# Kernel tuning notes

Measured on AMD Instinct MI355X. Metric: run time of the kernel, lower is better.

Reference implementation:

```python
import jax, jax.numpy as jnp
import numpy as np

BS, SL, N_AGENTS, OBS_DIM, STATE_DIM, N_EDGES, HID = 32, 512, 32, 96, 1024, 64, 256


def _hgcn(w_line, x, H):
    # x: [B, n, 1]; H: [B, n, E]. Faithful to torch HGCN:
    # A = D^{-1/2} H |W| B^{-1} H^T D^{-1/2}, with D, B built from detached H/|W|,
    # inf entries (from 0^{-1} / 0^{-0.5}) zeroed. Diagonal matmuls are implicit scalings.
    w_abs = jnp.abs(w_line)
    Hd = jax.lax.stop_gradient(H)
    d = jnp.einsum('bne,e->bn', Hd, jax.lax.stop_gradient(w_abs))  # [B, n]
    d_is = jnp.where(d > 0, jax.lax.rsqrt(jnp.where(d > 0, d, 1.0)), 0.0)
    b = jnp.sum(Hd, axis=-2)  # [B, E]
    b_inv = jnp.where(b > 0, 1.0 / jnp.where(b > 0, b, 1.0), 0.0)
    t = d_is[..., None] * x                       # D^{-1/2} x
    s = jnp.einsum('bne,bnk->bek', H, t)          # H^T (...)
    s = s * (w_abs[None, :] * b_inv)[..., None]   # |W| B^{-1} (diagonals commute)
    y = jnp.einsum('bne,bek->bnk', H, s)          # H (...)
    return d_is[..., None] * y                    # D^{-1/2} (...)


def _mlp(x, w1, b1, w2, b2):
    return jax.nn.relu(x @ w1 + b1) @ w2 + b2


def setup_inputs() -> dict:
    key = jax.random.key(0)
    ks = jax.random.split(key, 24)
    f = jax.random.normal
    inp = {
        'agent_qs': f(ks[0], (BS, SL, N_AGENTS), jnp.float32),
        'states': f(ks[1], (BS, SL, STATE_DIM), jnp.float32),
        'indiv_us': f(ks[2], (BS, SL, N_AGENTS, OBS_DIM), jnp.float32),
        'edge_W': f(ks[3], (OBS_DIM, N_EDGES), jnp.float32) * 0.1,
        'edge_b': f(ks[4], (N_EDGES,), jnp.float32) * 0.1,
        'wline1': 1.0 + 0.1 * f(ks[5], (N_EDGES,), jnp.float32),
        'wline2': 1.0 + 0.1 * f(ks[6], (N_EDGES,), jnp.float32),
    }
    names = ['hw1', 'hc1', 'hw', 'hc']
    outs = [N_AGENTS, N_AGENTS, N_AGENTS, 1]
    for i, (nm, od) in enumerate(zip(names, outs)):
        inp[nm + '_w1'] = f(ks[7 + 4 * i], (STATE_DIM, HID), jnp.float32) * 0.05
        inp[nm + '_b1'] = f(ks[8 + 4 * i], (HID,), jnp.float32) * 0.05
        inp[nm + '_w2'] = f(ks[9 + 4 * i], (HID, od), jnp.float32) * 0.05
        inp[nm + '_b2'] = f(ks[10 + 4 * i], (od,), jnp.float32) * 0.05
    return inp


def reference(agent_qs, states, indiv_us, edge_W, edge_b, wline1, wline2,
              hw1_w1, hw1_b1, hw1_w2, hw1_b2, hc1_w1, hc1_b1, hc1_w2, hc1_b2,
              hw_w1, hw_b1, hw_w2, hw_b2, hc_w1, hc_b1, hc_w2, hc_b2):
    bs, sl, n = agent_qs.shape
    q = agent_qs.reshape(-1, n)                               # [B, n]
    u = indiv_us.reshape(-1, n, indiv_us.shape[-1])           # [B, n, obs]
    s = states.reshape(-1, states.shape[-1])                  # [B, state_dim]
    H = jax.nn.relu(u @ edge_W + edge_b)                      # hyper_edge_net -> [B, n, E]
    x = q[..., None]                                          # node_features [B, n, 1]
    qs_tot = _hgcn(wline2, _hgcn(wline1, x, H), H)[..., 0]    # two stacked HGCN encoders
    w1 = jnp.abs(_mlp(s, hw1_w1, hw1_b1, hw1_w2, hw1_b2))
    c1 = _mlp(s, hc1_w1, hc1_b1, hc1_w2, hc1_b2)
    qt = jax.nn.elu(qs_tot * w1 + c1)
    w = jnp.abs(_mlp(s, hw_w1, hw_b1, hw_w2, hw_b2))
    c = _mlp(s, hc_w1, hc_b1, hc_w2, hc_b2)[..., 0]
    q_tot = jnp.sum(qt * w, axis=-1) + c
    return q_tot.reshape(bs, sl, 1)
```

## Files before the change

### kernel.cpp

```cpp
#include <hip/hip_runtime.h>
#include <cstdint>

typedef _Float16 f16;
typedef _Float16 f16x4 __attribute__((ext_vector_type(4)));
typedef _Float16 f16x8 __attribute__((ext_vector_type(8)));
typedef float f32x4 __attribute__((ext_vector_type(4)));

#define AS1U const __attribute__((address_space(1))) unsigned int
#define AS3U __attribute__((address_space(3))) unsigned int

__device__ __forceinline__ void gload_lds16(const void* g, void* l) {
    __builtin_amdgcn_global_load_lds((AS1U*)g, (AS3U*)l, 16, 0, 0);
}

#define WSYNC() asm volatile("s_waitcnt lgkmcnt(0)" ::: "memory")

#define BATCH 16384
#define NAG   32
#define OBS   96
#define SDIM  1024
#define NE    64
#define HIDN  256
#define NH    1024

#define NB_ST 1024
#define NB_PW 256
#define NB_SM 101
#define NB_HG 4096
#define NB_FRONT (NB_ST + NB_PW + NB_SM + NB_HG)

__global__ __launch_bounds__(256) void k_front(
    const float* __restrict__ agent_qs, const float* __restrict__ states,
    const float* __restrict__ indiv_us, const float* __restrict__ edge_W,
    const float* __restrict__ edge_b, const float* __restrict__ wline1,
    const float* __restrict__ wline2,
    const float* __restrict__ w1a, const float* __restrict__ w1b,
    const float* __restrict__ w1c, const float* __restrict__ w1d,
    const float* __restrict__ b1a, const float* __restrict__ b1b,
    const float* __restrict__ b1c, const float* __restrict__ b1d,
    const float* __restrict__ w2a, const float* __restrict__ w2b,
    const float* __restrict__ w2c, const float* __restrict__ w2d,
    f16* __restrict__ states16, f16* __restrict__ W1t, float* __restrict__ b1cat,
    f16* __restrict__ W2t, f16* __restrict__ hcw2, float* __restrict__ qs_tot) {
    __shared__ __align__(16) char arena[50688];
    const int tid = threadIdx.x;
    int bid = blockIdx.x;

    if (bid < NB_ST) {
        int i = bid * 256 + tid;
        const int n4 = BATCH * SDIM / 4;
        const int stride = NB_ST * 256;
        for (; i < n4; i += stride) {
            float4 v = ((const float4*)states)[i];
            f16x4 h = { (f16)v.x, (f16)v.y, (f16)v.z, (f16)v.w };
            ((f16x4*)states16)[i] = h;
        }
        return;
    }
    bid -= NB_ST;
    if (bid < NB_PW) {
        float* tile = (float*)arena;
        int mlp = bid >> 6, rem = bid & 63, kt = rem >> 2, ct = rem & 3;
        const float* src = (mlp == 0) ? w1a : (mlp == 1) ? w1b : (mlp == 2) ? w1c : w1d;
        int k0 = kt * 64, c0 = ct * 64;
        for (int i = tid; i < 4096; i += 256) {
            int kk = i >> 6, cc = i & 63;
            tile[kk * 65 + cc] = src[(size_t)(k0 + kk) * 256 + c0 + cc];
        }
        __syncthreads();
        for (int i = tid; i < 4096; i += 256) {
            int cc = i >> 6, kk = i & 63;
            W1t[(size_t)(mlp * 256 + c0 + cc) * 1024 + k0 + kk] = (f16)tile[kk * 65 + cc];
        }
        return;
    }
    bid -= NB_PW;
    if (bid < NB_SM) {
        int i = bid * 256 + tid;
        if (i < 24576) {
            int mp = i >> 13, rem = i & 8191, oo = rem >> 8, kk = rem & 255;
            const float* src = (mp == 0) ? w2a : (mp == 1) ? w2b : w2c;
            W2t[i] = (f16)src[kk * 32 + oo];
        } else if (i < 24832) {
            int k = i - 24576;
            hcw2[k] = (f16)w2d[k];
        } else {
            int n = i - 24832;
            int mlp = n >> 8, c = n & 255;
            const float* bsrc = (mlp == 0) ? b1a : (mlp == 1) ? b1b : (mlp == 2) ? b1c : b1d;
            b1cat[n] = bsrc[c];
        }
        return;
    }
    bid -= NB_SM;

    f16*   eWs   = (f16*)arena;
    float* swa   = (float*)(arena + 13312);
    float* HsB   = (float*)(arena + 13824);
    float* svB   = (float*)(arena + 47104);
    float* sttB  = (float*)(arena + 48128);
    float* sdisB = (float*)(arena + 48640);
    float* sbinvB= (float*)(arena + 49664);

    const int w = tid >> 6, l = tid & 63;
    const int b = bid * 4 + w;
    float* Hw    = HsB + w * 2080;
    float* sv    = svB + w * 64;
    float* stt   = sttB + w * 32;
    float* sdis  = sdisB + w * 64;
    float* sbinv = sbinvB + w * 64;

    for (int i = tid; i < 6144; i += 256) {
        int k = i >> 6, n = i & 63;
        eWs[n * 104 + k] = (f16)edge_W[i];
    }
    if (tid < 64) swa[tid] = fabsf(wline1[tid]);
    else if (tid < 128) swa[tid] = fabsf(wline2[tid - 64]);
    __syncthreads();

    const int lm = l & 15, lk = l >> 4;
    const float* ub = indiv_us + (size_t)b * (NAG * OBS);

    #pragma unroll
    for (int mt = 0; mt < 2; mt++) {
        f16x8 af[3];
        #pragma unroll
        for (int ks = 0; ks < 3; ks++) {
            const float* up = ub + (mt * 16 + lm) * 96 + ks * 32 + lk * 8;
            float4 v0 = *(const float4*)up;
            float4 v1 = *(const float4*)(up + 4);
            af[ks] = (f16x8){ (f16)v0.x, (f16)v0.y, (f16)v0.z, (f16)v0.w,
                              (f16)v1.x, (f16)v1.y, (f16)v1.z, (f16)v1.w };
        }
        #pragma unroll
        for (int nt = 0; nt < 4; nt++) {
            f32x4 acc = {0.f, 0.f, 0.f, 0.f};
            #pragma unroll
            for (int ks = 0; ks < 3; ks++) {
                f16x8 bb = *(const f16x8*)&eWs[(nt * 16 + lm) * 104 + ks * 32 + lk * 8];
                acc = __builtin_amdgcn_mfma_f32_16x16x32_f16(af[ks], bb, acc, 0, 0, 0);
            }
            int col = nt * 16 + lm;
            float bias = edge_b[col];
            #pragma unroll
            for (int r = 0; r < 4; r++) {
                int row = mt * 16 + lk * 4 + r;
                float hv = acc[r] + bias;
                Hw[row * 65 + col] = hv > 0.f ? hv : 0.f;
            }
        }
    }
    WSYNC();

    float bsum = 0.f;
    #pragma unroll
    for (int n = 0; n < 32; n++) bsum += Hw[n * 65 + l];
    sbinv[l] = bsum > 0.f ? 1.f / bsum : 0.f;

    const int nn = l & 31, half = l >> 5;
    float dd = 0.f;
    #pragma unroll 8
    for (int e = 0; e < 64; e++) dd += Hw[nn * 65 + e] * swa[half * 64 + e];
    float dis = dd > 0.f ? rsqrtf(dd) : 0.f;
    sdis[l] = dis;
    float q = agent_qs[(size_t)b * 32 + nn];
    if (half == 0) stt[nn] = dis * q;
    WSYNC();

    float s1 = 0.f;
    #pragma unroll
    for (int n = 0; n < 32; n++) s1 += Hw[n * 65 + l] * stt[n];
    sv[l] = s1 * swa[l] * sbinv[l];
    WSYNC();

    float y1 = 0.f;
    #pragma unroll 8
    for (int e = 0; e < 64; e++) y1 += Hw[nn * 65 + e] * sv[e];
    float x2 = sdis[nn] * y1;
    if (half == 0) stt[nn] = sdis[32 + nn] * x2;
    WSYNC();

    float s2 = 0.f;
    #pragma unroll
    for (int n = 0; n < 32; n++) s2 += Hw[n * 65 + l] * stt[n];
    sv[l] = s2 * swa[64 + l] * sbinv[l];
    WSYNC();

    float y2 = 0.f;
    #pragma unroll 8
    for (int e = 0; e < 64; e++) y2 += Hw[nn * 65 + e] * sv[e];
    if (half == 0) qs_tot[(size_t)b * 32 + nn] = sdis[32 + nn] * y2;
}

__global__ __launch_bounds__(256) void k_gemm1(
    const f16* __restrict__ A, const f16* __restrict__ B,
    const float* __restrict__ b1cat, const f16* __restrict__ W2t,
    const f16* __restrict__ hcw2, float* __restrict__ Pp) {
    __shared__ __align__(16) char smem[33792];
    f16* As = (f16*)smem;
    f16* Bs = (f16*)(smem + 16384);
    f16* Ts = (f16*)smem;

    const int tid = threadIdx.x;
    const int w = tid >> 6, l = tid & 63;
    const int p = blockIdx.x;
    const int xcd = p & 7, slot = p >> 3;
    const int region = slot >> 6, rs = slot & 63;
    const int mt = (xcd * 2 + region) * 8 + (rs >> 3);
    const int nt = rs & 7;
    const int m0 = mt * 128, n0 = nt * 128;
    const int wm = w >> 1, wn = w & 1;
    const int lm = l & 15, lk = l >> 4;
    const int srow = l >> 3;
    const int scol = (l & 7) * 8;

    f32x4 acc[4][4];
    #pragma unroll
    for (int i = 0; i < 4; i++)
        #pragma unroll
        for (int j = 0; j < 4; j++) acc[i][j] = (f32x4){0.f, 0.f, 0.f, 0.f};

    for (int kt = 0; kt < 16; kt++) {
        #pragma unroll
        for (int i = 0; i < 4; i++) {
            int c = w * 4 + i;
            int row = c * 8 + srow;
            gload_lds16(&A[(size_t)(m0 + row) * 1024 + kt * 64 + scol], &As[c * 512]);
            gload_lds16(&B[(size_t)(n0 + row) * 1024 + kt * 64 + scol], &Bs[c * 512]);
        }
        __syncthreads();
        #pragma unroll
        for (int ks = 0; ks < 2; ks++) {
            f16x8 a[4], bb[4];
            #pragma unroll
            for (int i = 0; i < 4; i++)
                a[i] = *(const f16x8*)&As[(wm * 64 + i * 16 + lm) * 64 + ks * 32 + lk * 8];
            #pragma unroll
            for (int j = 0; j < 4; j++)
                bb[j] = *(const f16x8*)&Bs[(wn * 64 + j * 16 + lm) * 64 + ks * 32 + lk * 8];
            #pragma unroll
            for (int i = 0; i < 4; i++)
                #pragma unroll
                for (int j = 0; j < 4; j++)
                    acc[i][j] = __builtin_amdgcn_mfma_f32_16x16x32_f16(a[i], bb[j], acc[i][j], 0, 0, 0);
        }
        __syncthreads();
    }

    float bj[4];
    #pragma unroll
    for (int j = 0; j < 4; j++) bj[j] = b1cat[n0 + wn * 64 + j * 16 + lm];
    #pragma unroll
    for (int i = 0; i < 4; i++)
        #pragma unroll
        for (int r = 0; r < 4; r++) {
            int row = wm * 64 + i * 16 + lk * 4 + r;
            #pragma unroll
            for (int j = 0; j < 4; j++) {
                int col = wn * 64 + j * 16 + lm;
                float v = acc[i][j][r] + bj[j];
                Ts[row * 132 + col] = (f16)(v > 0.f ? v : 0.f);
            }
        }
    __syncthreads();

    const int mlp = nt >> 1, kh = nt & 1;
    const int rbase = w * 32;
    if (mlp < 3) {
        const f16* wb = W2t + mlp * 8192 + kh * 128;
        f32x4 acc2[2][2];
        acc2[0][0] = (f32x4){0,0,0,0}; acc2[0][1] = (f32x4){0,0,0,0};
        acc2[1][0] = (f32x4){0,0,0,0}; acc2[1][1] = (f32x4){0,0,0,0};
        #pragma unroll
        for (int ks = 0; ks < 4; ks++) {
            f16x8 b0 = *(const f16x8*)&wb[lm * 256 + ks * 32 + lk * 8];
            f16x8 b1 = *(const f16x8*)&wb[(16 + lm) * 256 + ks * 32 + lk * 8];
            #pragma unroll
            for (int i2 = 0; i2 < 2; i2++) {
                f16x8 a = *(const f16x8*)&Ts[(rbase + i2 * 16 + lm) * 132 + ks * 32 + lk * 8];
                acc2[i2][0] = __builtin_amdgcn_mfma_f32_16x16x32_f16(a, b0, acc2[i2][0], 0, 0, 0);
                acc2[i2][1] = __builtin_amdgcn_mfma_f32_16x16x32_f16(a, b1, acc2[i2][1], 0, 0, 0);
            }
        }
        #pragma unroll
        for (int i2 = 0; i2 < 2; i2++)
            #pragma unroll
            for (int j2 = 0; j2 < 2; j2++)
                #pragma unroll
                for (int r = 0; r < 4; r++)
                    Pp[((size_t)kh * BATCH + m0 + rbase + i2 * 16 + lk * 4 + r) * 104
                       + mlp * 32 + j2 * 16 + lm] = acc2[i2][j2][r];
    } else {
        const f16* hc = hcw2 + kh * 128;
        f32x4 acc2[2];
        acc2[0] = (f32x4){0,0,0,0}; acc2[1] = (f32x4){0,0,0,0};
        #pragma unroll
        for (int ks = 0; ks < 4; ks++) {
            f16x8 bz = (f16x8){0,0,0,0,0,0,0,0};
            if (lm == 0) bz = *(const f16x8*)&hc[ks * 32 + lk * 8];
            #pragma unroll
            for (int i2 = 0; i2 < 2; i2++) {
                f16x8 a = *(const f16x8*)&Ts[(rbase + i2 * 16 + lm) * 132 + ks * 32 + lk * 8];
                acc2[i2] = __builtin_amdgcn_mfma_f32_16x16x32_f16(a, bz, acc2[i2], 0, 0, 0);
            }
        }
        if (lm == 0)
            #pragma unroll
            for (int i2 = 0; i2 < 2; i2++)
                #pragma unroll
                for (int r = 0; r < 4; r++)
                    Pp[((size_t)kh * BATCH + m0 + rbase + i2 * 16 + lk * 4 + r) * 104 + 96]
                        = acc2[i2][r];
    }
}

__global__ __launch_bounds__(256) void k_ep(
    const float* __restrict__ Pp, const float* __restrict__ qs_tot,
    const float* __restrict__ hw1_b2, const float* __restrict__ hc1_b2,
    const float* __restrict__ hw_b2, const float* __restrict__ hc_b2,
    float* __restrict__ out) {
    const int tid = threadIdx.x;
    const int row = blockIdx.x * 32 + (tid >> 3);
    const int q8 = tid & 7, o = q8 * 4;
    const float* p0 = Pp + (size_t)row * 104;
    const float* p1 = Pp + (size_t)(BATCH + row) * 104;
    f32x4 a0 = *(const f32x4*)(p0 + o);
    f32x4 a1 = *(const f32x4*)(p1 + o);
    f32x4 c0 = *(const f32x4*)(p0 + 32 + o);
    f32x4 c1 = *(const f32x4*)(p1 + 32 + o);
    f32x4 w0 = *(const f32x4*)(p0 + 64 + o);
    f32x4 w1 = *(const f32x4*)(p1 + 64 + o);
    f32x4 qs = *(const f32x4*)(qs_tot + (size_t)row * 32 + o);
    float val = 0.f;
    #pragma unroll
    for (int j = 0; j < 4; j++) {
        float wv1 = fabsf(a0[j] + a1[j] + hw1_b2[o + j]);
        float cv1 = c0[j] + c1[j] + hc1_b2[o + j];
        float wv  = fabsf(w0[j] + w1[j] + hw_b2[o + j]);
        float z = qs[j] * wv1 + cv1;
        float qt = z > 0.f ? z : expm1f(z);
        val += qt * wv;
    }
    val += __shfl_xor(val, 1);
    val += __shfl_xor(val, 2);
    val += __shfl_xor(val, 4);
    if (q8 == 0) out[row] = val + p0[96] + p1[96] + hc_b2[0];
}

extern "C" void kernel_launch(void* const* d_in, const int* in_sizes, int n_in,
                              void* d_out, int out_size, void* d_ws, size_t ws_size,
                              hipStream_t stream) {
    const float* agent_qs = (const float*)d_in[0];
    const float* states   = (const float*)d_in[1];
    const float* indiv_us = (const float*)d_in[2];
    const float* edge_W   = (const float*)d_in[3];
    const float* edge_b   = (const float*)d_in[4];
    const float* wline1   = (const float*)d_in[5];
    const float* wline2   = (const float*)d_in[6];
    const float* hw1_w1 = (const float*)d_in[7];
    const float* hw1_b1 = (const float*)d_in[8];
    const float* hw1_w2 = (const float*)d_in[9];
    const float* hw1_b2 = (const float*)d_in[10];
    const float* hc1_w1 = (const float*)d_in[11];
    const float* hc1_b1 = (const float*)d_in[12];
    const float* hc1_w2 = (const float*)d_in[13];
    const float* hc1_b2 = (const float*)d_in[14];
    const float* hw_w1  = (const float*)d_in[15];
    const float* hw_b1  = (const float*)d_in[16];
    const float* hw_w2  = (const float*)d_in[17];
    const float* hw_b2  = (const float*)d_in[18];
    const float* hc_w1  = (const float*)d_in[19];
    const float* hc_b1  = (const float*)d_in[20];
    const float* hc_w2  = (const float*)d_in[21];
    const float* hc_b2  = (const float*)d_in[22];

    char* ws = (char*)d_ws;
    size_t o_states16 = 0;
    size_t o_qs   = o_states16 + (size_t)BATCH * SDIM * 2;
    size_t o_W1t  = o_qs + (size_t)BATCH * NAG * 4;
    size_t o_b1   = o_W1t + (size_t)NH * SDIM * 2;
    size_t o_W2t  = o_b1 + 4096;
    size_t o_hcw2 = o_W2t + 49152;
    size_t o_Pp   = o_hcw2 + 512;

    f16*   states16 = (f16*)(ws + o_states16);
    float* qs_tot   = (float*)(ws + o_qs);
    f16*   W1t      = (f16*)(ws + o_W1t);
    float* b1cat    = (float*)(ws + o_b1);
    f16*   W2t      = (f16*)(ws + o_W2t);
    f16*   hcw2     = (f16*)(ws + o_hcw2);
    float* Pp       = (float*)(ws + o_Pp);

    k_front<<<NB_FRONT, 256, 0, stream>>>(
        agent_qs, states, indiv_us, edge_W, edge_b, wline1, wline2,
        hw1_w1, hc1_w1, hw_w1, hc_w1, hw1_b1, hc1_b1, hw_b1, hc_b1,
        hw1_w2, hc1_w2, hw_w2, hc_w2,
        states16, W1t, b1cat, W2t, hcw2, qs_tot);
    k_gemm1<<<1024, 256, 0, stream>>>(states16, W1t, b1cat, W2t, hcw2, Pp);
    k_ep<<<BATCH / 32, 256, 0, stream>>>(Pp, qs_tot, hw1_b2, hc1_b2, hw_b2, hc_b2,
                                         (float*)d_out);
}
```

Baseline: 144.3 us.

## Fuse states fp16 conversion into GEMM and co-schedule HGCN blocks with GEMM blocks

Removes the separate pass that converted states to fp16 in a workspace buffer. The GEMM now loads fp32 states directly and converts them in registers before a swizzled LDS store. The weight-prep work moves to a small preceding kernel, and the GEMM and HGCN blocks are interleaved in one launch (one GEMM block per five). This is meant to cut the states round trip and overlap compute-bound GEMM with the memory-bound HGCN. In exchange, the GEMM A-operand loads are no longer async global-to-LDS, and an XOR swizzle is added to avoid LDS bank conflicts.

```diff
diff --git a/kernel.cpp b/kernel.cpp
--- a/kernel.cpp
+++ b/kernel.cpp
@@ -23,43 +23,28 @@
 #define HIDN  256
 #define NH    1024
 
-#define NB_ST 1024
-#define NB_PW 256
-#define NB_SM 101
-#define NB_HG 4096
-#define NB_FRONT (NB_ST + NB_PW + NB_SM + NB_HG)
-
-__global__ __launch_bounds__(256) void k_front(
-    const float* __restrict__ agent_qs, const float* __restrict__ states,
-    const float* __restrict__ indiv_us, const float* __restrict__ edge_W,
-    const float* __restrict__ edge_b, const float* __restrict__ wline1,
-    const float* __restrict__ wline2,
+#define NB_PW   256
+#define NB_SM   101
+#define NB_PREP (NB_PW + NB_SM)
+
+#define NB_GEMM 1024
+#define NB_HG   4096
+#define NB_MAIN 5120
+
+__global__ __launch_bounds__(256) void k_prep(
     const float* __restrict__ w1a, const float* __restrict__ w1b,
     const float* __restrict__ w1c, const float* __restrict__ w1d,
     const float* __restrict__ b1a, const float* __restrict__ b1b,
     const float* __restrict__ b1c, const float* __restrict__ b1d,
     const float* __restrict__ w2a, const float* __restrict__ w2b,
     const float* __restrict__ w2c, const float* __restrict__ w2d,
-    f16* __restrict__ states16, f16* __restrict__ W1t, float* __restrict__ b1cat,
-    f16* __restrict__ W2t, f16* __restrict__ hcw2, float* __restrict__ qs_tot) {
-    __shared__ __align__(16) char arena[50688];
+    f16* __restrict__ W1t, float* __restrict__ b1cat,
+    f16* __restrict__ W2t, f16* __restrict__ hcw2) {
+    __shared__ float tile[64 * 65];
     const int tid = threadIdx.x;
     int bid = blockIdx.x;
 
-    if (bid < NB_ST) {
-        int i = bid * 256 + tid;
-        const int n4 = BATCH * SDIM / 4;
-        const int stride = NB_ST * 256;
-        for (; i < n4; i += stride) {
-            float4 v = ((const float4*)states)[i];
-            f16x4 h = { (f16)v.x, (f16)v.y, (f16)v.z, (f16)v.w };
-            ((f16x4*)states16)[i] = h;
-        }
-        return;
-    }
-    bid -= NB_ST;
     if (bid < NB_PW) {
-        float* tile = (float*)arena;
         int mlp = bid >> 6, rem = bid & 63, kt = rem >> 2, ct = rem & 3;
         const float* src = (mlp == 0) ? w1a : (mlp == 1) ? w1b : (mlp == 2) ? w1c : w1d;
         int k0 = kt * 64, c0 = ct * 64;
@@ -75,24 +60,164 @@
         return;
     }
     bid -= NB_PW;
-    if (bid < NB_SM) {
-        int i = bid * 256 + tid;
-        if (i < 24576) {
-            int mp = i >> 13, rem = i & 8191, oo = rem >> 8, kk = rem & 255;
-            const float* src = (mp == 0) ? w2a : (mp == 1) ? w2b : w2c;
-            W2t[i] = (f16)src[kk * 32 + oo];
-        } else if (i < 24832) {
-            int k = i - 24576;
-            hcw2[k] = (f16)w2d[k];
+    int i = bid * 256 + tid;
+    if (i < 24576) {
+        int mp = i >> 13, rem = i & 8191, oo = rem >> 8, kk = rem & 255;
+        const float* src = (mp == 0) ? w2a : (mp == 1) ? w2b : w2c;
+        W2t[i] = (f16)src[kk * 32 + oo];
+    } else if (i < 24832) {
+        int k = i - 24576;
+        hcw2[k] = (f16)w2d[k];
+    } else {
+        int n = i - 24832;
+        int mlp = n >> 8, c = n & 255;
+        const float* bsrc = (mlp == 0) ? b1a : (mlp == 1) ? b1b : (mlp == 2) ? b1c : b1d;
+        b1cat[n] = bsrc[c];
+    }
+}
+
+__global__ __launch_bounds__(256) void k_main(
+    const float* __restrict__ agent_qs, const float* __restrict__ states,
+    const float* __restrict__ indiv_us, const float* __restrict__ edge_W,
+    const float* __restrict__ edge_b, const float* __restrict__ wline1,
+    const float* __restrict__ wline2,
+    const f16* __restrict__ W1t, const float* __restrict__ b1cat,
+    const f16* __restrict__ W2t, const f16* __restrict__ hcw2,
+    float* __restrict__ qs_tot, float* __restrict__ Pp) {
+    __shared__ __align__(16) char arena[50688];
+    const int tid = threadIdx.x;
+    const int bid = blockIdx.x;
+    const int w = tid >> 6, l = tid & 63;
+    const int lm = l & 15, lk = l >> 4;
+
+    if (bid % 5 == 0) {
+        f16* As = (f16*)arena;
+        f16* Bs = (f16*)(arena + 16384);
+        f16* Ts = (f16*)arena;
+
+        const int g = bid / 5;
+        const int xcd = bid & 7;
+        const int slot = g >> 3;
+        const int region = slot >> 5;
+        const int rs = slot & 31;
+        const int mt = (xcd * 4 + region) * 4 + (rs >> 3);
+        const int nt = rs & 7;
+        const int m0 = mt * 128, n0 = nt * 128;
+        const int wm = w >> 1, wn = w & 1;
+        const int srow = l >> 3, schunk = l & 7;
+        const int gchunk = schunk ^ srow;
+
+        f32x4 acc[4][4];
+        #pragma unroll
+        for (int i = 0; i < 4; i++)
+            #pragma unroll
+            for (int j = 0; j < 4; j++) acc[i][j] = (f32x4){0.f, 0.f, 0.f, 0.f};
+
+        for (int kt = 0; kt < 16; kt++) {
+            #pragma unroll
+            for (int i = 0; i < 4; i++) {
+                int c = w * 4 + i;
+                int row = c * 8 + srow;
+                gload_lds16(&W1t[(size_t)(n0 + row) * 1024 + kt * 64 + gchunk * 8], &Bs[c * 512]);
+            }
+            #pragma unroll
+            for (int i = 0; i < 4; i++) {
+                int idx = i * 256 + tid;
+                int row = idx >> 3, ch = idx & 7;
+                const float* src = &states[(size_t)(m0 + row) * 1024 + kt * 64 + ch * 8];
+                float4 v0 = *(const float4*)src;
+                float4 v1 = *(const float4*)(src + 4);
+                f16x8 hv = { (f16)v0.x, (f16)v0.y, (f16)v0.z, (f16)v0.w,
+                             (f16)v1.x, (f16)v1.y, (f16)v1.z, (f16)v1.w };
+                *(f16x8*)&As[row * 64 + ((ch ^ (row & 7)) << 3)] = hv;
+            }
+            __syncthreads();
+            #pragma unroll
+            for (int ks = 0; ks < 2; ks++) {
+                const int sw = ((ks * 4 + lk) ^ (lm & 7)) << 3;
+                f16x8 a[4], bb[4];
+                #pragma unroll
+                for (int i = 0; i < 4; i++)
+                    a[i] = *(const f16x8*)&As[(wm * 64 + i * 16 + lm) * 64 + sw];
+                #pragma unroll
+                for (int j = 0; j < 4; j++)
+                    bb[j] = *(const f16x8*)&Bs[(wn * 64 + j * 16 + lm) * 64 + sw];
+                #pragma unroll
+                for (int i = 0; i < 4; i++)
+                    #pragma unroll
+                    for (int j = 0; j < 4; j++)
+                        acc[i][j] = __builtin_amdgcn_mfma_f32_16x16x32_f16(a[i], bb[j], acc[i][j], 0, 0, 0);
+            }
+            __syncthreads();
+        }
+
+        float bj[4];
+        #pragma unroll
+        for (int j = 0; j < 4; j++) bj[j] = b1cat[n0 + wn * 64 + j * 16 + lm];
+        #pragma unroll
+        for (int i = 0; i < 4; i++)
+            #pragma unroll
+            for (int r = 0; r < 4; r++) {
+                int row = wm * 64 + i * 16 + lk * 4 + r;
+                #pragma unroll
+                for (int j = 0; j < 4; j++) {
+                    int col = wn * 64 + j * 16 + lm;
+                    float v = acc[i][j][r] + bj[j];
+                    Ts[row * 132 + col] = (f16)(v > 0.f ? v : 0.f);
+                }
+            }
+        __syncthreads();
+
+        const int mlp = nt >> 1, kh = nt & 1;
+        const int rbase = w * 32;
+        if (mlp < 3) {
+            const f16* wb = W2t + mlp * 8192 + kh * 128;
+            f32x4 acc2[2][2];
+            acc2[0][0] = (f32x4){0,0,0,0}; acc2[0][1] = (f32x4){0,0,0,0};
+            acc2[1][0] = (f32x4){0,0,0,0}; acc2[1][1] = (f32x4){0,0,0,0};
+            #pragma unroll
+            for (int ks = 0; ks < 4; ks++) {
+                f16x8 b0 = *(const f16x8*)&wb[lm * 256 + ks * 32 + lk * 8];
+                f16x8 b1 = *(const f16x8*)&wb[(16 + lm) * 256 + ks * 32 + lk * 8];
+                #pragma unroll
+                for (int i2 = 0; i2 < 2; i2++) {
+                    f16x8 a = *(const f16x8*)&Ts[(rbase + i2 * 16 + lm) * 132 + ks * 32 + lk * 8];
+                    acc2[i2][0] = __builtin_amdgcn_mfma_f32_16x16x32_f16(a, b0, acc2[i2][0], 0, 0, 0);
+                    acc2[i2][1] = __builtin_amdgcn_mfma_f32_16x16x32_f16(a, b1, acc2[i2][1], 0, 0, 0);
+                }
+            }
+            #pragma unroll
+            for (int i2 = 0; i2 < 2; i2++)
+                #pragma unroll
+                for (int j2 = 0; j2 < 2; j2++)
+                    #pragma unroll
+                    for (int r = 0; r < 4; r++)
+                        Pp[((size_t)kh * BATCH + m0 + rbase + i2 * 16 + lk * 4 + r) * 104
+                           + mlp * 32 + j2 * 16 + lm] = acc2[i2][j2][r];
         } else {
-            int n = i - 24832;
-            int mlp = n >> 8, c = n & 255;
-            const float* bsrc = (mlp == 0) ? b1a : (mlp == 1) ? b1b : (mlp == 2) ? b1c : b1d;
-            b1cat[n] = bsrc[c];
+            const f16* hc = hcw2 + kh * 128;
+            f32x4 acc2[2];
+            acc2[0] = (f32x4){0,0,0,0}; acc2[1] = (f32x4){0,0,0,0};
+            #pragma unroll
+            for (int ks = 0; ks < 4; ks++) {
+                f16x8 bz = (f16x8){0,0,0,0,0,0,0,0};
+                if (lm == 0) bz = *(const f16x8*)&hc[ks * 32 + lk * 8];
+                #pragma unroll
+                for (int i2 = 0; i2 < 2; i2++) {
+                    f16x8 a = *(const f16x8*)&Ts[(rbase + i2 * 16 + lm) * 132 + ks * 32 + lk * 8];
+                    acc2[i2] = __builtin_amdgcn_mfma_f32_16x16x32_f16(a, bz, acc2[i2], 0, 0, 0);
+                }
+            }
+            if (lm == 0)
+                #pragma unroll
+                for (int i2 = 0; i2 < 2; i2++)
+                    #pragma unroll
+                    for (int r = 0; r < 4; r++)
+                        Pp[((size_t)kh * BATCH + m0 + rbase + i2 * 16 + lk * 4 + r) * 104 + 96]
+                            = acc2[i2][r];
         }
         return;
     }
-    bid -= NB_SM;
 
     f16*   eWs   = (f16*)arena;
     float* swa   = (float*)(arena + 13312);
@@ -102,8 +227,8 @@
     float* sdisB = (float*)(arena + 48640);
     float* sbinvB= (float*)(arena + 49664);
 
-    const int w = tid >> 6, l = tid & 63;
-    const int b = bid * 4 + w;
+    const int hbid = 4 * (bid / 5) + (bid % 5) - 1;
+    const int b = hbid * 4 + w;
     float* Hw    = HsB + w * 2080;
     float* sv    = svB + w * 64;
     float* stt   = sttB + w * 32;
@@ -118,7 +243,6 @@
     else if (tid < 128) swa[tid] = fabsf(wline2[tid - 64]);
     __syncthreads();
 
-    const int lm = l & 15, lk = l >> 4;
     const float* ub = indiv_us + (size_t)b * (NAG * OBS);
 
     #pragma unroll
@@ -190,128 +314,6 @@
     #pragma unroll 8
     for (int e = 0; e < 64; e++) y2 += Hw[nn * 65 + e] * sv[e];
     if (half == 0) qs_tot[(size_t)b * 32 + nn] = sdis[32 + nn] * y2;
-}
-
-__global__ __launch_bounds__(256) void k_gemm1(
-    const f16* __restrict__ A, const f16* __restrict__ B,
-    const float* __restrict__ b1cat, const f16* __restrict__ W2t,
-    const f16* __restrict__ hcw2, float* __restrict__ Pp) {
-    __shared__ __align__(16) char smem[33792];
-    f16* As = (f16*)smem;
-    f16* Bs = (f16*)(smem + 16384);
-    f16* Ts = (f16*)smem;
-
-    const int tid = threadIdx.x;
-    const int w = tid >> 6, l = tid & 63;
-    const int p = blockIdx.x;
-    const int xcd = p & 7, slot = p >> 3;
-    const int region = slot >> 6, rs = slot & 63;
-    const int mt = (xcd * 2 + region) * 8 + (rs >> 3);
-    const int nt = rs & 7;
-    const int m0 = mt * 128, n0 = nt * 128;
-    const int wm = w >> 1, wn = w & 1;
-    const int lm = l & 15, lk = l >> 4;
-    const int srow = l >> 3;
-    const int scol = (l & 7) * 8;
-
-    f32x4 acc[4][4];
-    #pragma unroll
-    for (int i = 0; i < 4; i++)
-        #pragma unroll
-        for (int j = 0; j < 4; j++) acc[i][j] = (f32x4){0.f, 0.f, 0.f, 0.f};
-
-    for (int kt = 0; kt < 16; kt++) {
-        #pragma unroll
-        for (int i = 0; i < 4; i++) {
-            int c = w * 4 + i;
-            int row = c * 8 + srow;
-            gload_lds16(&A[(size_t)(m0 + row) * 1024 + kt * 64 + scol], &As[c * 512]);
-            gload_lds16(&B[(size_t)(n0 + row) * 1024 + kt * 64 + scol], &Bs[c * 512]);
-        }
-        __syncthreads();
-        #pragma unroll
-        for (int ks = 0; ks < 2; ks++) {
-            f16x8 a[4], bb[4];
-            #pragma unroll
-            for (int i = 0; i < 4; i++)
-                a[i] = *(const f16x8*)&As[(wm * 64 + i * 16 + lm) * 64 + ks * 32 + lk * 8];
-            #pragma unroll
-            for (int j = 0; j < 4; j++)
-                bb[j] = *(const f16x8*)&Bs[(wn * 64 + j * 16 + lm) * 64 + ks * 32 + lk * 8];
-            #pragma unroll
-            for (int i = 0; i < 4; i++)
-                #pragma unroll
-                for (int j = 0; j < 4; j++)
-                    acc[i][j] = __builtin_amdgcn_mfma_f32_16x16x32_f16(a[i], bb[j], acc[i][j], 0, 0, 0);
-        }
-        __syncthreads();
-    }
-
-    float bj[4];
-    #pragma unroll
-    for (int j = 0; j < 4; j++) bj[j] = b1cat[n0 + wn * 64 + j * 16 + lm];
-    #pragma unroll
-    for (int i = 0; i < 4; i++)
-        #pragma unroll
-        for (int r = 0; r < 4; r++) {
-            int row = wm * 64 + i * 16 + lk * 4 + r;
-            #pragma unroll
-            for (int j = 0; j < 4; j++) {
-                int col = wn * 64 + j * 16 + lm;
-                float v = acc[i][j][r] + bj[j];
-                Ts[row * 132 + col] = (f16)(v > 0.f ? v : 0.f);
-            }
-        }
-    __syncthreads();
-
-    const int mlp = nt >> 1, kh = nt & 1;
-    const int rbase = w * 32;
-    if (mlp < 3) {
-        const f16* wb = W2t + mlp * 8192 + kh * 128;
-        f32x4 acc2[2][2];
-        acc2[0][0] = (f32x4){0,0,0,0}; acc2[0][1] = (f32x4){0,0,0,0};
-        acc2[1][0] = (f32x4){0,0,0,0}; acc2[1][1] = (f32x4){0,0,0,0};
-        #pragma unroll
-        for (int ks = 0; ks < 4; ks++) {
-            f16x8 b0 = *(const f16x8*)&wb[lm * 256 + ks * 32 + lk * 8];
-            f16x8 b1 = *(const f16x8*)&wb[(16 + lm) * 256 + ks * 32 + lk * 8];
-            #pragma unroll
-            for (int i2 = 0; i2 < 2; i2++) {
-                f16x8 a = *(const f16x8*)&Ts[(rbase + i2 * 16 + lm) * 132 + ks * 32 + lk * 8];
-                acc2[i2][0] = __builtin_amdgcn_mfma_f32_16x16x32_f16(a, b0, acc2[i2][0], 0, 0, 0);
-                acc2[i2][1] = __builtin_amdgcn_mfma_f32_16x16x32_f16(a, b1, acc2[i2][1], 0, 0, 0);
-            }
-        }
-        #pragma unroll
-        for (int i2 = 0; i2 < 2; i2++)
-            #pragma unroll
-            for (int j2 = 0; j2 < 2; j2++)
-                #pragma unroll
-                for (int r = 0; r < 4; r++)
-                    Pp[((size_t)kh * BATCH + m0 + rbase + i2 * 16 + lk * 4 + r) * 104
-                       + mlp * 32 + j2 * 16 + lm] = acc2[i2][j2][r];
-    } else {
-        const f16* hc = hcw2 + kh * 128;
-        f32x4 acc2[2];
-        acc2[0] = (f32x4){0,0,0,0}; acc2[1] = (f32x4){0,0,0,0};
-        #pragma unroll
-        for (int ks = 0; ks < 4; ks++) {
-            f16x8 bz = (f16x8){0,0,0,0,0,0,0,0};
-            if (lm == 0) bz = *(const f16x8*)&hc[ks * 32 + lk * 8];
-            #pragma unroll
-            for (int i2 = 0; i2 < 2; i2++) {
-                f16x8 a = *(const f16x8*)&Ts[(rbase + i2 * 16 + lm) * 132 + ks * 32 + lk * 8];
-                acc2[i2] = __builtin_amdgcn_mfma_f32_16x16x32_f16(a, bz, acc2[i2], 0, 0, 0);
-            }
-        }
-        if (lm == 0)
-            #pragma unroll
-            for (int i2 = 0; i2 < 2; i2++)
-                #pragma unroll
-                for (int r = 0; r < 4; r++)
-                    Pp[((size_t)kh * BATCH + m0 + rbase + i2 * 16 + lk * 4 + r) * 104 + 96]
-                        = acc2[i2][r];
-    }
 }
 
 __global__ __launch_bounds__(256) void k_ep(
@@ -375,15 +377,13 @@
     const float* hc_b2  = (const float*)d_in[22];
 
     char* ws = (char*)d_ws;
-    size_t o_states16 = 0;
-    size_t o_qs   = o_states16 + (size_t)BATCH * SDIM * 2;
+    size_t o_qs   = 0;
     size_t o_W1t  = o_qs + (size_t)BATCH * NAG * 4;
     size_t o_b1   = o_W1t + (size_t)NH * SDIM * 2;
     size_t o_W2t  = o_b1 + 4096;
     size_t o_hcw2 = o_W2t + 49152;
     size_t o_Pp   = o_hcw2 + 512;
 
-    f16*   states16 = (f16*)(ws + o_states16);
     float* qs_tot   = (float*)(ws + o_qs);
     f16*   W1t      = (f16*)(ws + o_W1t);
     float* b1cat    = (float*)(ws + o_b1);
@@ -391,12 +391,12 @@
     f16*   hcw2     = (f16*)(ws + o_hcw2);
     float* Pp       = (float*)(ws + o_Pp);
 
-    k_front<<<NB_FRONT, 256, 0, stream>>>(
+    k_prep<<<NB_PREP, 256, 0, stream>>>(
+        hw1_w1, hc1_w1, hw_w1, hc_w1, hw1_b1, hc1_b1, hw_b1, hc_b1,
+        hw1_w2, hc1_w2, hw_w2, hc_w2, W1t, b1cat, W2t, hcw2);
+    k_main<<<NB_MAIN, 256, 0, stream>>>(
         agent_qs, states, indiv_us, edge_W, edge_b, wline1, wline2,
-        hw1_w1, hc1_w1, hw_w1, hc_w1, hw1_b1, hc1_b1, hw_b1, hc_b1,
-        hw1_w2, hc1_w2, hw_w2, hc_w2,
-        states16, W1t, b1cat, W2t, hcw2, qs_tot);
-    k_gemm1<<<1024, 256, 0, stream>>>(states16, W1t, b1cat, W2t, hcw2, Pp);
+        W1t, b1cat, W2t, hcw2, qs_tot, Pp);
     k_ep<<<BATCH / 32, 256, 0, stream>>>(Pp, qs_tot, hw1_b2, hc1_b2, hw_b2, hc_b2,
                                          (float*)d_out);
 }
```

Result: slower. 171.6 us (+19.0%).
